# Kernel tuning notes

Hardware: AMD Instinct MI355X
Metric: run time of the kernel (lower is better)

Reference implementation:

```python
import jax, jax.numpy as jnp
import numpy as np

K = 6  # knn_number
EPS_CS = 1e-8  # F.cosine_similarity eps


def _sqdist(a, b):
    # a: [B,N,3], b: [B,M,3] -> [B,N,M] squared euclidean distances
    return (jnp.sum(a * a, -1)[:, :, None]
            + jnp.sum(b * b, -1)[:, None, :]
            - 2.0 * jnp.einsum('bnc,bmc->bnm', a, b))


def _batch_norm(x):
    # normalize last dim with the module's exact epsilons
    n = jnp.sqrt(jnp.sum(x * x, axis=-1, keepdims=True) + 1e-08)
    return x / (n + 1e-10)


def _cossim(a, b):
    # torch F.cosine_similarity semantics along last dim
    na = jnp.maximum(jnp.sqrt(jnp.sum(a * a, -1)), EPS_CS)
    nb = jnp.maximum(jnp.sqrt(jnp.sum(b * b, -1)), EPS_CS)
    return jnp.sum(a * b, -1) / (na * nb)


def _gather(points, idx):
    # points: [B,N,C], idx: [B,...] int -> [B,...,C]
    return jax.vmap(lambda p, i: p[i])(points, idx)


def _avg_ori(group_ori, group_nor, batch_ori, batch_nor):
    # group_*: [B,N,K,3], batch_*: [B,N,3]
    nor_diff = jnp.sum(group_nor * batch_nor[:, :, None, :], axis=3)  # [B,N,K]
    nor_diff = jnp.exp(-nor_diff / 0.3) * 10.0 + 1.0
    nor_diff = jnp.where(nor_diff < 4.0, 1.0, 5.0)
    batch_ori_rot = jnp.cross(batch_ori, batch_nor)  # get_ori_rot90: ori x nor
    cos0 = _cossim(group_ori, batch_ori[:, :, None, :])       # [B,N,K]
    cos1 = _cossim(group_ori, batch_ori_rot[:, :, None, :])   # [B,N,K]
    cos = jnp.minimum(1.0 - jnp.abs(cos0), 1.0 - jnp.abs(cos1))
    return jnp.mean(nor_diff * cos)


def _forward(ori_pre, nor_pre, xyz_up, xyz_offset, pts, gt):
    ori_pre = _batch_norm(ori_pre)
    nor_pre = _batch_norm(nor_pre)
    xyz_gt = gt[:, :, 0:3]
    xyz_nor = gt[:, :, 3:6]

    # ori-loss: NN of pts in gt, gather gt normals
    index = jnp.argmin(_sqdist(pts, xyz_gt), axis=2)  # [B,N]
    nor_gt = _gather(xyz_nor, index)                  # [B,N,3]
    d_n = jnp.sum(nor_gt * ori_pre, axis=2, keepdims=True)
    ori_pro = _batch_norm(ori_pre - nor_gt * d_n)

    # smooth field over KNN (self-knn over pts, includes self)
    idx = jax.lax.top_k(-_sqdist(pts, pts), K)[1]  # [B,N,K]
    group_ori = _gather(ori_pro, idx)              # [B,N,K,3]
    group_nor = _gather(nor_gt, idx)
    loss_smooth = _avg_ori(group_ori, group_nor, ori_pro, nor_gt)

    # normal estimation loss
    loss_nor = jnp.mean(1.0 - jnp.abs(_cossim(nor_gt, nor_pre)))

    # chamfer distances (squared-dist chamfer)
    do = _sqdist(xyz_offset, xyz_gt)
    loss_charm_offset = jnp.mean(jnp.min(do, axis=2)) + jnp.mean(jnp.min(do, axis=1))
    du = _sqdist(xyz_up, xyz_gt)
    loss_charm = jnp.mean(jnp.min(du, axis=2)) + jnp.mean(jnp.min(du, axis=1))

    # nor-ori orthogonality
    loss_nor_ori = jnp.mean(jnp.abs(jnp.sum(ori_pre * nor_gt, axis=2)))

    loss_cd = loss_charm + 0.4 * loss_charm_offset
    loss = loss_smooth + loss_nor + 0.1 * loss_nor_ori + 200.0 * loss_cd
    return (loss, loss_smooth, loss_nor, loss_charm_offset, loss_nor_ori, loss_charm, loss_charm)


def setup_inputs() -> dict:
    key = jax.random.key(0)
    k = jax.random.split(key, 6)
    B, N, NG, NU = 4, 4096, 4096, 8192
    gt_xyz = jax.random.normal(k[5], (B, NG, 3), dtype=jnp.float32)
    gt_nor = _batch_norm(jax.random.normal(jax.random.fold_in(key, 7), (B, NG, 3), dtype=jnp.float32))
    return {
        'ori_pre': jax.random.normal(k[0], (B, N, 3), dtype=jnp.float32),
        'nor_pre': jax.random.normal(k[1], (B, N, 3), dtype=jnp.float32),
        'xyz_up': jax.random.normal(k[2], (B, NU, 3), dtype=jnp.float32),
        'xyz_offset': jax.random.normal(k[3], (B, NU, 3), dtype=jnp.float32),
        'pts': jax.random.normal(k[4], (B, N, 3), dtype=jnp.float32),
        'gt': jnp.concatenate([gt_xyz, gt_nor], axis=-1),
        'epoch': 1,
    }


def reference(ori_pre, nor_pre, xyz_up, xyz_offset, pts, gt, epoch):
    # epoch is unused by the original forward as well
    return _forward(ori_pre, nor_pre, xyz_up, xyz_offset, pts, gt)
```

## Files before the change

### kernel.cpp

```cpp
#include <hip/hip_runtime.h>
#include <stdint.h>

#define NN 4096
#define NGG 4096
#define NUU 8192

__device__ __forceinline__ unsigned fkey32(float f) {
  unsigned u = __float_as_uint(f);
  return u ^ (((int)u >> 31) | 0x80000000u);
}
__device__ __forceinline__ float unfkey32(unsigned k) {
  unsigned m = (k & 0x80000000u) ? 0x80000000u : 0xFFFFFFFFu;
  return __uint_as_float(k ^ m);
}

__device__ __forceinline__ float block_sum_256(float v, float* sbuf) {
#pragma unroll
  for (int o = 32; o > 0; o >>= 1) v += __shfl_down(v, o, 64);
  int lane = threadIdx.x & 63;
  int w = threadIdx.x >> 6;
  if (lane == 0) sbuf[w] = v;
  __syncthreads();
  float r = 0.f;
  if (threadIdx.x == 0) r = sbuf[0] + sbuf[1] + sbuf[2] + sbuf[3];
  __syncthreads();
  return r;
}

__device__ __forceinline__ float block_sum_512(float v, float* sbuf) {
#pragma unroll
  for (int o = 32; o > 0; o >>= 1) v += __shfl_down(v, o, 64);
  int lane = threadIdx.x & 63;
  int w = threadIdx.x >> 6;
  if (lane == 0) sbuf[w] = v;
  __syncthreads();
  float r = 0.f;
  if (threadIdx.x == 0) {
#pragma unroll
    for (int i = 0; i < 8; ++i) r += sbuf[i];
  }
  __syncthreads();
  return r;
}

__global__ __launch_bounds__(256) void k_scan(const float* __restrict__ pts,
                                              const float* __restrict__ gt,
                                              const float* __restrict__ up,
                                              const float* __restrict__ off,
                                              unsigned long long* __restrict__ keys,
                                              unsigned* __restrict__ rowmin,
                                              unsigned* __restrict__ colmin,
                                              float* __restrict__ acc) {
  __shared__ float4 sc[512];
  int blk = blockIdx.x;
  int tid = threadIdx.x;
  if (blk == 0 && tid < 16) acc[tid] = 0.f;

  if (blk < 512) {
    int qb = blk >> 3;
    int seg = blk & 7;
    int wb = qb >> 3;
    int which = wb >> 2;
    int b = wb & 3;
    int r0 = (qb & 7) * 1024 + tid * 4;
    {
      const float* gtb = gt + (size_t)b * NGG * 6 + (size_t)seg * 512 * 6;
      int i0 = tid * 2;
      const float4* g4 = (const float4*)(gtb + (size_t)i0 * 6);
      float4 u0 = g4[0], u1 = g4[1], u2 = g4[2];
      sc[i0] = make_float4(u0.x, u0.y, u0.z,
                           fmaf(u0.x, u0.x, fmaf(u0.y, u0.y, u0.z * u0.z)));
      sc[i0 + 1] = make_float4(u1.z, u1.w, u2.x,
                               fmaf(u1.z, u1.z, fmaf(u1.w, u1.w, u2.x * u2.x)));
    }
    const float* src = which ? up : off;
    const float4* s4 = (const float4*)src;
    size_t fb = ((size_t)(b * NUU + r0) * 3) >> 2;
    float4 A = s4[fb], B = s4[fb + 1], C = s4[fb + 2];
    float q0x = A.x, q0y = A.y, q0z = A.z;
    float q1x = A.w, q1y = B.x, q1z = B.y;
    float q2x = B.z, q2y = B.w, q2z = C.x;
    float q3x = C.y, q3y = C.z, q3z = C.w;
    float qq0 = fmaf(q0x, q0x, fmaf(q0y, q0y, q0z * q0z));
    float qq1 = fmaf(q1x, q1x, fmaf(q1y, q1y, q1z * q1z));
    float qq2 = fmaf(q2x, q2x, fmaf(q2y, q2y, q2z * q2z));
    float qq3 = fmaf(q3x, q3x, fmaf(q3y, q3y, q3z * q3z));
    float a0x = -2.f * q0x, a0y = -2.f * q0y, a0z = -2.f * q0z;
    float a1x = -2.f * q1x, a1y = -2.f * q1y, a1z = -2.f * q1z;
    float a2x = -2.f * q2x, a2y = -2.f * q2y, a2z = -2.f * q2z;
    float a3x = -2.f * q3x, a3y = -2.f * q3y, a3z = -2.f * q3z;
    __syncthreads();
    float b0 = 3.4e38f, b1 = 3.4e38f, b2 = 3.4e38f, b3 = 3.4e38f;
#pragma unroll 4
    for (int j = 0; j < 512; ++j) {
      float4 c = sc[j];
      float t;
      t = fmaf(c.x, a0x, c.w); t = fmaf(c.y, a0y, t); t = fmaf(c.z, a0z, t); b0 = fminf(b0, t);
      t = fmaf(c.x, a1x, c.w); t = fmaf(c.y, a1y, t); t = fmaf(c.z, a1z, t); b1 = fminf(b1, t);
      t = fmaf(c.x, a2x, c.w); t = fmaf(c.y, a2y, t); t = fmaf(c.z, a2z, t); b2 = fminf(b2, t);
      t = fmaf(c.x, a3x, c.w); t = fmaf(c.y, a3y, t); t = fmaf(c.z, a3z, t); b3 = fminf(b3, t);
    }
    int gr = which * 32768 + b * NUU + r0;
    atomicMin(&rowmin[gr + 0], fkey32(b0 + qq0));
    atomicMin(&rowmin[gr + 1], fkey32(b1 + qq1));
    atomicMin(&rowmin[gr + 2], fkey32(b2 + qq2));
    atomicMin(&rowmin[gr + 3], fkey32(b3 + qq3));

  } else if (blk < 1024) {
    int blk2 = blk - 512;
    int qb = blk2 >> 4;
    int seg = blk2 & 15;
    int which = qb >> 4;
    int b = (qb >> 2) & 3;
    int m0 = (qb & 3) * 1024 + tid * 4;
    const float* src = which ? up : off;
    if (tid < 128) {
      const float* sb = src + (size_t)b * NUU * 3 + (size_t)seg * 512 * 3;
      int i0 = tid * 4;
      const float4* s4 = (const float4*)(sb + (size_t)i0 * 3);
      float4 u0 = s4[0], u1 = s4[1], u2 = s4[2];
      sc[i0] = make_float4(u0.x, u0.y, u0.z,
                           fmaf(u0.x, u0.x, fmaf(u0.y, u0.y, u0.z * u0.z)));
      sc[i0 + 1] = make_float4(u0.w, u1.x, u1.y,
                               fmaf(u0.w, u0.w, fmaf(u1.x, u1.x, u1.y * u1.y)));
      sc[i0 + 2] = make_float4(u1.z, u1.w, u2.x,
                               fmaf(u1.z, u1.z, fmaf(u1.w, u1.w, u2.x * u2.x)));
      sc[i0 + 3] = make_float4(u2.y, u2.z, u2.w,
                               fmaf(u2.y, u2.y, fmaf(u2.z, u2.z, u2.w * u2.w)));
    }
    const float* g = gt + (size_t)b * NGG * 6 + (size_t)m0 * 6;
    float q0x = g[0],  q0y = g[1],  q0z = g[2];
    float q1x = g[6],  q1y = g[7],  q1z = g[8];
    float q2x = g[12], q2y = g[13], q2z = g[14];
    float q3x = g[18], q3y = g[19], q3z = g[20];
    float qq0 = fmaf(q0x, q0x, fmaf(q0y, q0y, q0z * q0z));
    float qq1 = fmaf(q1x, q1x, fmaf(q1y, q1y, q1z * q1z));
    float qq2 = fmaf(q2x, q2x, fmaf(q2y, q2y, q2z * q2z));
    float qq3 = fmaf(q3x, q3x, fmaf(q3y, q3y, q3z * q3z));
    float a0x = -2.f * q0x, a0y = -2.f * q0y, a0z = -2.f * q0z;
    float a1x = -2.f * q1x, a1y = -2.f * q1y, a1z = -2.f * q1z;
    float a2x = -2.f * q2x, a2y = -2.f * q2y, a2z = -2.f * q2z;
    float a3x = -2.f * q3x, a3y = -2.f * q3y, a3z = -2.f * q3z;
    __syncthreads();
    float b0 = 3.4e38f, b1 = 3.4e38f, b2 = 3.4e38f, b3 = 3.4e38f;
#pragma unroll 4
    for (int j = 0; j < 512; ++j) {
      float4 c = sc[j];
      float t;
      t = fmaf(c.x, a0x, c.w); t = fmaf(c.y, a0y, t); t = fmaf(c.z, a0z, t); b0 = fminf(b0, t);
      t = fmaf(c.x, a1x, c.w); t = fmaf(c.y, a1y, t); t = fmaf(c.z, a1z, t); b1 = fminf(b1, t);
      t = fmaf(c.x, a2x, c.w); t = fmaf(c.y, a2y, t); t = fmaf(c.z, a2z, t); b2 = fminf(b2, t);
      t = fmaf(c.x, a3x, c.w); t = fmaf(c.y, a3y, t); t = fmaf(c.z, a3z, t); b3 = fminf(b3, t);
    }
    int gc = which * 16384 + b * NGG + m0;
    atomicMin(&colmin[gc + 0], fkey32(b0 + qq0));
    atomicMin(&colmin[gc + 1], fkey32(b1 + qq1));
    atomicMin(&colmin[gc + 2], fkey32(b2 + qq2));
    atomicMin(&colmin[gc + 3], fkey32(b3 + qq3));

  } else {
    int blk3 = blk - 1024;
    int qb = blk3 >> 4;
    int seg = blk3 & 15;
    int b = qb >> 2;
    int m0 = (qb & 3) * 1024 + tid * 4;
    if (tid < 128) {
      const float* gtb = gt + (size_t)b * NGG * 6 + (size_t)seg * 256 * 6;
      int i0 = tid * 2;
      const float4* g4 = (const float4*)(gtb + (size_t)i0 * 6);
      float4 u0 = g4[0], u1 = g4[1], u2 = g4[2];
      sc[i0] = make_float4(u0.x, u0.y, u0.z,
                           fmaf(u0.x, u0.x, fmaf(u0.y, u0.y, u0.z * u0.z)));
      sc[i0 + 1] = make_float4(u1.z, u1.w, u2.x,
                               fmaf(u1.z, u1.z, fmaf(u1.w, u1.w, u2.x * u2.x)));
    }
    size_t fb = ((size_t)(b * NN + m0) * 3) >> 2;
    const float4* p4 = (const float4*)pts;
    float4 A = p4[fb], B = p4[fb + 1], C = p4[fb + 2];
    float q0x = A.x, q0y = A.y, q0z = A.z;
    float q1x = A.w, q1y = B.x, q1z = B.y;
    float q2x = B.z, q2y = B.w, q2z = C.x;
    float q3x = C.y, q3y = C.z, q3z = C.w;
    float a0x = -2.f * q0x, a0y = -2.f * q0y, a0z = -2.f * q0z;
    float a1x = -2.f * q1x, a1y = -2.f * q1y, a1z = -2.f * q1z;
    float a2x = -2.f * q2x, a2y = -2.f * q2y, a2z = -2.f * q2z;
    float a3x = -2.f * q3x, a3y = -2.f * q3y, a3z = -2.f * q3z;
    __syncthreads();
    float b0 = 3.4e38f, b1 = 3.4e38f, b2 = 3.4e38f, b3 = 3.4e38f;
    int i0 = 0, i1 = 0, i2 = 0, i3 = 0;
#pragma unroll 4
    for (int j = 0; j < 256; ++j) {
      float4 c = sc[j];
      float t; bool cc;
      t = fmaf(c.x, a0x, c.w); t = fmaf(c.y, a0y, t); t = fmaf(c.z, a0z, t);
      cc = t < b0; b0 = cc ? t : b0; i0 = cc ? j : i0;
      t = fmaf(c.x, a1x, c.w); t = fmaf(c.y, a1y, t); t = fmaf(c.z, a1z, t);
      cc = t < b1; b1 = cc ? t : b1; i1 = cc ? j : i1;
      t = fmaf(c.x, a2x, c.w); t = fmaf(c.y, a2y, t); t = fmaf(c.z, a2z, t);
      cc = t < b2; b2 = cc ? t : b2; i2 = cc ? j : i2;
      t = fmaf(c.x, a3x, c.w); t = fmaf(c.y, a3y, t); t = fmaf(c.z, a3z, t);
      cc = t < b3; b3 = cc ? t : b3; i3 = cc ? j : i3;
    }
    int q = b * NN + m0;
    int base = seg * 256;
    atomicMin(&keys[q + 0], ((unsigned long long)fkey32(b0) << 32) | (unsigned)(base + i0));
    atomicMin(&keys[q + 1], ((unsigned long long)fkey32(b1) << 32) | (unsigned)(base + i1));
    atomicMin(&keys[q + 2], ((unsigned long long)fkey32(b2) << 32) | (unsigned)(base + i2));
    atomicMin(&keys[q + 3], ((unsigned long long)fkey32(b3) << 32) | (unsigned)(base + i3));
  }
}

__global__ __launch_bounds__(256) void k_post(
    const float* __restrict__ ori_pre, const float* __restrict__ nor_pre,
    const float* __restrict__ gt, const unsigned long long* __restrict__ keys,
    const unsigned* __restrict__ rowmin, const unsigned* __restrict__ colmin,
    float* __restrict__ nor_gt, float* __restrict__ ori_pro, float* __restrict__ acc) {
  __shared__ float sb1[4], sb2[4];
  int blk = blockIdx.x;
  if (blk < 64) {
    int q = blk * 256 + threadIdx.x;
    int b = q >> 12;
    float ox = ori_pre[q * 3 + 0], oy = ori_pre[q * 3 + 1], oz = ori_pre[q * 3 + 2];
    float n1 = sqrtf(fmaf(ox, ox, fmaf(oy, oy, oz * oz)) + 1e-8f) + 1e-10f;
    ox /= n1; oy /= n1; oz /= n1;
    float px = nor_pre[q * 3 + 0], py = nor_pre[q * 3 + 1], pz = nor_pre[q * 3 + 2];
    float n2 = sqrtf(fmaf(px, px, fmaf(py, py, pz * pz)) + 1e-8f) + 1e-10f;
    px /= n2; py /= n2; pz /= n2;
    unsigned idx = (unsigned)(keys[q] & 0xffffffffULL);
    const float* g = gt + (size_t)b * NGG * 6 + (size_t)idx * 6 + 3;
    float gx = g[0], gy = g[1], gz = g[2];
    float dn = fmaf(gx, ox, fmaf(gy, oy, gz * oz));
    float vx = ox - gx * dn, vy = oy - gy * dn, vz = oz - gz * dn;
    float n3 = sqrtf(fmaf(vx, vx, fmaf(vy, vy, vz * vz)) + 1e-8f) + 1e-10f;
    vx /= n3; vy /= n3; vz /= n3;
    nor_gt[q * 3 + 0] = gx; nor_gt[q * 3 + 1] = gy; nor_gt[q * 3 + 2] = gz;
    ori_pro[q * 3 + 0] = vx; ori_pro[q * 3 + 1] = vy; ori_pro[q * 3 + 2] = vz;
    float na = fmaxf(sqrtf(fmaf(gx, gx, fmaf(gy, gy, gz * gz))), 1e-8f);
    float nb = fmaxf(sqrtf(fmaf(px, px, fmaf(py, py, pz * pz))), 1e-8f);
    float cs = fmaf(gx, px, fmaf(gy, py, gz * pz)) / (na * nb);
    float t_nor = 1.f - fabsf(cs);
    float t_ori = fabsf(dn);
    float s1 = block_sum_256(t_nor, sb1);
    float s2 = block_sum_256(t_ori, sb2);
    if (threadIdx.x == 0) {
      atomicAdd(&acc[1], s1);
      atomicAdd(&acc[2], s2);
    }
  } else {
    int rblk = blk - 64;
    float v;
    int slot;
    if (rblk < 256) {
      int i = rblk * 256 + threadIdx.x;
      v = unfkey32(rowmin[i]);
      slot = (i >> 15) ? 5 : 3;
    } else {
      int i = (rblk - 256) * 256 + threadIdx.x;
      v = unfkey32(colmin[i]);
      slot = (i >> 14) ? 6 : 4;
    }
    float s = block_sum_256(v, sb1);
    if (threadIdx.x == 0) atomicAdd(&acc[slot], s);
  }
}

#define INSERT6(D, CI)                                                          \
  {                                                                             \
    float d_ = (D); int ci_ = (CI);                                             \
    bool cc; float nd; int ni;                                                  \
    cc = d_ < d0; nd = cc ? d_ : d0; d_ = cc ? d0 : d_; ni = cc ? ci_ : i0; ci_ = cc ? i0 : ci_; d0 = nd; i0 = ni; \
    cc = d_ < d1; nd = cc ? d_ : d1; d_ = cc ? d1 : d_; ni = cc ? ci_ : i1; ci_ = cc ? i1 : ci_; d1 = nd; i1 = ni; \
    cc = d_ < d2; nd = cc ? d_ : d2; d_ = cc ? d2 : d_; ni = cc ? ci_ : i2; ci_ = cc ? i2 : ci_; d2 = nd; i2 = ni; \
    cc = d_ < d3; nd = cc ? d_ : d3; d_ = cc ? d3 : d_; ni = cc ? ci_ : i3; ci_ = cc ? i3 : ci_; d3 = nd; i3 = ni; \
    cc = d_ < d4; nd = cc ? d_ : d4; d_ = cc ? d4 : d_; ni = cc ? ci_ : i4; ci_ = cc ? i4 : ci_; d4 = nd; i4 = ni; \
    cc = d_ < d5; nd = cc ? d_ : d5;                    ni = cc ? ci_ : i5;                      d5 = nd; i5 = ni; \
  }

__global__ __launch_bounds__(512, 8) void k_knn_smooth(const float* __restrict__ pts,
                                                       const float* __restrict__ nor_gt,
                                                       const float* __restrict__ ori_pro,
                                                       float* __restrict__ acc,
                                                       float* __restrict__ out) {
  __shared__ float4 sp[1152];
  __shared__ float sbuf[8];
  int tid = threadIdx.x;
  int q_local = tid >> 5;
  int t = tid & 31;
  int q = blockIdx.x * 16 + q_local;
  int b = q >> 12;
  int n = q & 4095;
  const float* pb = pts + (size_t)b * NN * 3;
  float qx = pb[n * 3 + 0], qy = pb[n * 3 + 1], qz = pb[n * 3 + 2];
  float qx2 = -2.f * qx, qy2 = -2.f * qy, qz2 = -2.f * qz;
  float d0 = 3.4e38f, d1 = 3.4e38f, d2 = 3.4e38f,
        d3 = 3.4e38f, d4 = 3.4e38f, d5 = 3.4e38f;
  int i0 = 0, i1 = 0, i2 = 0, i3 = 0, i4 = 0, i5 = 0;
  int toff = t + (t >> 3);

  for (int ch = 0; ch < 4; ++ch) {
    if (tid < 256) {
      const float4* p4 = (const float4*)(pb + (size_t)(ch * 1024 + tid * 4) * 3);
      float4 u0 = p4[0], u1 = p4[1], u2 = p4[2];
      int il = tid * 4;
      int si = il + (il >> 3);
      sp[si] = make_float4(u0.x, u0.y, u0.z,
                           fmaf(u0.x, u0.x, fmaf(u0.y, u0.y, u0.z * u0.z)));
      sp[si + 1] = make_float4(u0.w, u1.x, u1.y,
                               fmaf(u0.w, u0.w, fmaf(u1.x, u1.x, u1.y * u1.y)));
      sp[si + 2] = make_float4(u1.z, u1.w, u2.x,
                               fmaf(u1.z, u1.z, fmaf(u1.w, u1.w, u2.x * u2.x)));
      sp[si + 3] = make_float4(u2.y, u2.z, u2.w,
                               fmaf(u2.y, u2.y, fmaf(u2.z, u2.z, u2.w * u2.w)));
    }
    __syncthreads();
    int cbase = ch << 10;
    for (int jo = 0; jo < 4; ++jo) {
      float T = d5;
#pragma unroll
      for (int o = 16; o > 0; o >>= 1) T = fminf(T, __shfl_xor(T, o, 32));
#pragma unroll
      for (int ji = 0; ji < 2; ++ji) {
        int c0 = (((jo << 1) | ji) << 7) | t;
        int s0 = c0 + (c0 >> 3);
        float4 p0 = sp[s0];
        float4 p1 = sp[s0 + 36];
        float4 p2 = sp[s0 + 72];
        float4 p3 = sp[s0 + 108];
        float da = fmaf(p0.x, qx2, p0.w); da = fmaf(p0.y, qy2, da); da = fmaf(p0.z, qz2, da);
        float db = fmaf(p1.x, qx2, p1.w); db = fmaf(p1.y, qy2, db); db = fmaf(p1.z, qz2, db);
        float dc = fmaf(p2.x, qx2, p2.w); dc = fmaf(p2.y, qy2, dc); dc = fmaf(p2.z, qz2, dc);
        float dd = fmaf(p3.x, qx2, p3.w); dd = fmaf(p3.y, qy2, dd); dd = fmaf(p3.z, qz2, dd);
        float mmin = fminf(fminf(da, db), fminf(dc, dd));
        if (mmin <= T) {
          int cg = cbase | c0;
          if (da <= T) INSERT6(da, cg)
          if (db <= T) INSERT6(db, cg + 32)
          if (dc <= T) INSERT6(dc, cg + 64)
          if (dd <= T) INSERT6(dd, cg + 96)
        }
      }
    }
    __syncthreads();
  }
  (void)toff;

  int myid = 0;
#pragma unroll
  for (int r = 0; r < 6; ++r) {
    unsigned long long h = ((unsigned long long)fkey32(d0) << 32) | (unsigned)i0;
    unsigned long long m = h;
#pragma unroll
    for (int o = 16; o > 0; o >>= 1) {
      unsigned long long other = __shfl_xor(m, o, 32);
      m = (other < m) ? other : m;
    }
    if (t == r) myid = (int)(m & 0xffffffffULL);
    if (h == m) {
      d0 = d1; i0 = i1; d1 = d2; i1 = i2; d2 = d3; i2 = i3;
      d3 = d4; i3 = i4; d4 = d5; i4 = i5; d5 = 3.4e38f;
    }
  }

  float sum = 0.f;
  if (t < 6) {
    const float* gq = nor_gt + (size_t)q * 3;
    float ngx = gq[0], ngy = gq[1], ngz = gq[2];
    const float* oq = ori_pro + (size_t)q * 3;
    float box = oq[0], boy = oq[1], boz = oq[2];
    float rx = boy * ngz - boz * ngy;
    float ry = boz * ngx - box * ngz;
    float rz = box * ngy - boy * ngx;
    float nbo = fmaxf(sqrtf(fmaf(box, box, fmaf(boy, boy, boz * boz))), 1e-8f);
    float nrot = fmaxf(sqrtf(fmaf(rx, rx, fmaf(ry, ry, rz * rz))), 1e-8f);
    const float* gn = nor_gt + (size_t)(b * 4096 + myid) * 3;
    const float* go = ori_pro + (size_t)(b * 4096 + myid) * 3;
    float gnx = gn[0], gny = gn[1], gnz = gn[2];
    float gox = go[0], goy = go[1], goz = go[2];
    float ndv = fmaf(gnx, ngx, fmaf(gny, ngy, gnz * ngz));
    float wv = (expf(-ndv / 0.3f) * 10.f + 1.f) < 4.f ? 1.f : 5.f;
    float ngo = fmaxf(sqrtf(fmaf(gox, gox, fmaf(goy, goy, goz * goz))), 1e-8f);
    float c0 = fmaf(gox, box, fmaf(goy, boy, goz * boz)) / (ngo * nbo);
    float c1 = fmaf(gox, rx, fmaf(goy, ry, goz * rz)) / (ngo * nrot);
    float cosv = fminf(1.f - fabsf(c0), 1.f - fabsf(c1));
    sum = wv * cosv;
  }
  float s = block_sum_512(sum, sbuf);

  if (tid == 0) {
    atomicAdd(&acc[0], s);
    __threadfence();
    unsigned c = atomicAdd((unsigned*)(acc + 9), 1u);
    if (c == gridDim.x - 1) {
      __threadfence();
      float a0 = atomicAdd(&acc[0], 0.f);
      float a1 = atomicAdd(&acc[1], 0.f);
      float a2 = atomicAdd(&acc[2], 0.f);
      float a3 = atomicAdd(&acc[3], 0.f);
      float a4 = atomicAdd(&acc[4], 0.f);
      float a5 = atomicAdd(&acc[5], 0.f);
      float a6 = atomicAdd(&acc[6], 0.f);
      float loss_smooth = a0 / 98304.f;
      float loss_nor = a1 / 16384.f;
      float loss_nor_ori = a2 / 16384.f;
      float lco = a3 / 32768.f + a4 / 16384.f;
      float lc = a5 / 32768.f + a6 / 16384.f;
      float loss_cd = lc + 0.4f * lco;
      float loss = loss_smooth + loss_nor + 0.1f * loss_nor_ori + 200.f * loss_cd;
      out[0] = loss;
      out[1] = loss_smooth;
      out[2] = loss_nor;
      out[3] = lco;
      out[4] = loss_nor_ori;
      out[5] = lc;
      out[6] = lc;
    }
  }
}

extern "C" void kernel_launch(void* const* d_in, const int* in_sizes, int n_in,
                              void* d_out, int out_size, void* d_ws, size_t ws_size,
                              hipStream_t stream) {
  (void)in_sizes; (void)n_in; (void)out_size; (void)ws_size;
  const float* ori_pre = (const float*)d_in[0];
  const float* nor_pre = (const float*)d_in[1];
  const float* xyz_up = (const float*)d_in[2];
  const float* xyz_off = (const float*)d_in[3];
  const float* pts = (const float*)d_in[4];
  const float* gt = (const float*)d_in[5];
  float* out = (float*)d_out;
  char* ws = (char*)d_ws;

  float* acc = (float*)(ws + 0);
  unsigned long long* keys = (unsigned long long*)(ws + 512);
  unsigned* rowmin = (unsigned*)(ws + 512 + 131072);
  unsigned* colmin = (unsigned*)(ws + 512 + 131072 + 262144);
  float* nor_gt = (float*)(ws + 512 + 131072 + 262144 + 131072);
  float* ori_pro = (float*)(ws + 512 + 131072 + 262144 + 131072 + 196608);

  hipMemsetAsync(ws + 512, 0xFF, 131072 + 262144 + 131072, stream);

  k_scan<<<1280, 256, 0, stream>>>(pts, gt, xyz_up, xyz_off, keys, rowmin,
                                   colmin, acc);
  k_post<<<448, 256, 0, stream>>>(ori_pre, nor_pre, gt, keys, rowmin, colmin,
                                  nor_gt, ori_pro, acc);
  k_knn_smooth<<<1024, 512, 0, stream>>>(pts, nor_gt, ori_pro, acc, out);
}
```

Measured before the change: 194.1 us.

## Stage all points in LDS once and prefilter KNN with a two-pass threshold

Loads all 4096 points per batch into shared memory in a single stage instead of four chunked loads with barriers. A first pass computes each lane's minimum distance, and the sixth-smallest of those per-lane minima across the 32 lanes becomes a safe upper bound tau on the true 6th-nearest distance. A second pass then inserts only candidates at or below tau, cutting top-6 insertion work and the per-chunk shuffle threshold updates. The costs are computing every distance twice, a much larger LDS footprint (about 72KB per block), and lower occupancy, with the launch-bounds minimum blocks lowered from 8 to 4.

```diff
diff --git a/kernel.cpp b/kernel.cpp
--- a/kernel.cpp
+++ b/kernel.cpp
@@ -276,12 +276,12 @@
     cc = d_ < d5; nd = cc ? d_ : d5;                    ni = cc ? ci_ : i5;                      d5 = nd; i5 = ni; \
   }
 
-__global__ __launch_bounds__(512, 8) void k_knn_smooth(const float* __restrict__ pts,
+__global__ __launch_bounds__(512, 4) void k_knn_smooth(const float* __restrict__ pts,
                                                        const float* __restrict__ nor_gt,
                                                        const float* __restrict__ ori_pro,
                                                        float* __restrict__ acc,
                                                        float* __restrict__ out) {
-  __shared__ float4 sp[1152];
+  __shared__ float4 sp[4608];
   __shared__ float sbuf[8];
   int tid = threadIdx.x;
   int q_local = tid >> 5;
@@ -290,72 +290,96 @@
   int b = q >> 12;
   int n = q & 4095;
   const float* pb = pts + (size_t)b * NN * 3;
+
+  {
+    int il = tid * 8;
+    const float4* p4 = (const float4*)(pb + (size_t)il * 3);
+    float4 u0 = p4[0], u1 = p4[1], u2 = p4[2], u3 = p4[3], u4 = p4[4], u5 = p4[5];
+    int si = il + (il >> 3);
+    sp[si + 0] = make_float4(u0.x, u0.y, u0.z,
+                             fmaf(u0.x, u0.x, fmaf(u0.y, u0.y, u0.z * u0.z)));
+    sp[si + 1] = make_float4(u0.w, u1.x, u1.y,
+                             fmaf(u0.w, u0.w, fmaf(u1.x, u1.x, u1.y * u1.y)));
+    sp[si + 2] = make_float4(u1.z, u1.w, u2.x,
+                             fmaf(u1.z, u1.z, fmaf(u1.w, u1.w, u2.x * u2.x)));
+    sp[si + 3] = make_float4(u2.y, u2.z, u2.w,
+                             fmaf(u2.y, u2.y, fmaf(u2.z, u2.z, u2.w * u2.w)));
+    sp[si + 4] = make_float4(u3.x, u3.y, u3.z,
+                             fmaf(u3.x, u3.x, fmaf(u3.y, u3.y, u3.z * u3.z)));
+    sp[si + 5] = make_float4(u3.w, u4.x, u4.y,
+                             fmaf(u3.w, u3.w, fmaf(u4.x, u4.x, u4.y * u4.y)));
+    sp[si + 6] = make_float4(u4.z, u4.w, u5.x,
+                             fmaf(u4.z, u4.z, fmaf(u4.w, u4.w, u5.x * u5.x)));
+    sp[si + 7] = make_float4(u5.y, u5.z, u5.w,
+                             fmaf(u5.y, u5.y, fmaf(u5.z, u5.z, u5.w * u5.w)));
+  }
+  __syncthreads();
+
   float qx = pb[n * 3 + 0], qy = pb[n * 3 + 1], qz = pb[n * 3 + 2];
   float qx2 = -2.f * qx, qy2 = -2.f * qy, qz2 = -2.f * qz;
+
+  float m = 3.4e38f;
+#pragma unroll 4
+  for (int gg = 0; gg < 32; ++gg) {
+    int c0 = (gg << 7) | t;
+    int s0 = c0 + (c0 >> 3);
+    float4 p0 = sp[s0];
+    float4 p1 = sp[s0 + 36];
+    float4 p2 = sp[s0 + 72];
+    float4 p3 = sp[s0 + 108];
+    float da = fmaf(p0.x, qx2, p0.w); da = fmaf(p0.y, qy2, da); da = fmaf(p0.z, qz2, da);
+    float db = fmaf(p1.x, qx2, p1.w); db = fmaf(p1.y, qy2, db); db = fmaf(p1.z, qz2, db);
+    float dc = fmaf(p2.x, qx2, p2.w); dc = fmaf(p2.y, qy2, dc); dc = fmaf(p2.z, qz2, dc);
+    float dd = fmaf(p3.x, qx2, p3.w); dd = fmaf(p3.y, qy2, dd); dd = fmaf(p3.z, qz2, dd);
+    m = fminf(m, fminf(fminf(da, db), fminf(dc, dd)));
+  }
+
+  float mv = m, tau = 3.4e38f;
+#pragma unroll
+  for (int r = 0; r < 6; ++r) {
+    float w = mv;
+#pragma unroll
+    for (int o = 16; o > 0; o >>= 1) w = fminf(w, __shfl_xor(w, o, 32));
+    tau = w;
+    if (mv == w) mv = 3.4e38f;
+  }
+
   float d0 = 3.4e38f, d1 = 3.4e38f, d2 = 3.4e38f,
         d3 = 3.4e38f, d4 = 3.4e38f, d5 = 3.4e38f;
   int i0 = 0, i1 = 0, i2 = 0, i3 = 0, i4 = 0, i5 = 0;
-  int toff = t + (t >> 3);
-
-  for (int ch = 0; ch < 4; ++ch) {
-    if (tid < 256) {
-      const float4* p4 = (const float4*)(pb + (size_t)(ch * 1024 + tid * 4) * 3);
-      float4 u0 = p4[0], u1 = p4[1], u2 = p4[2];
-      int il = tid * 4;
-      int si = il + (il >> 3);
-      sp[si] = make_float4(u0.x, u0.y, u0.z,
-                           fmaf(u0.x, u0.x, fmaf(u0.y, u0.y, u0.z * u0.z)));
-      sp[si + 1] = make_float4(u0.w, u1.x, u1.y,
-                               fmaf(u0.w, u0.w, fmaf(u1.x, u1.x, u1.y * u1.y)));
-      sp[si + 2] = make_float4(u1.z, u1.w, u2.x,
-                               fmaf(u1.z, u1.z, fmaf(u1.w, u1.w, u2.x * u2.x)));
-      sp[si + 3] = make_float4(u2.y, u2.z, u2.w,
-                               fmaf(u2.y, u2.y, fmaf(u2.z, u2.z, u2.w * u2.w)));
-    }
-    __syncthreads();
-    int cbase = ch << 10;
-    for (int jo = 0; jo < 4; ++jo) {
-      float T = d5;
-#pragma unroll
-      for (int o = 16; o > 0; o >>= 1) T = fminf(T, __shfl_xor(T, o, 32));
-#pragma unroll
-      for (int ji = 0; ji < 2; ++ji) {
-        int c0 = (((jo << 1) | ji) << 7) | t;
-        int s0 = c0 + (c0 >> 3);
-        float4 p0 = sp[s0];
-        float4 p1 = sp[s0 + 36];
-        float4 p2 = sp[s0 + 72];
-        float4 p3 = sp[s0 + 108];
-        float da = fmaf(p0.x, qx2, p0.w); da = fmaf(p0.y, qy2, da); da = fmaf(p0.z, qz2, da);
-        float db = fmaf(p1.x, qx2, p1.w); db = fmaf(p1.y, qy2, db); db = fmaf(p1.z, qz2, db);
-        float dc = fmaf(p2.x, qx2, p2.w); dc = fmaf(p2.y, qy2, dc); dc = fmaf(p2.z, qz2, dc);
-        float dd = fmaf(p3.x, qx2, p3.w); dd = fmaf(p3.y, qy2, dd); dd = fmaf(p3.z, qz2, dd);
-        float mmin = fminf(fminf(da, db), fminf(dc, dd));
-        if (mmin <= T) {
-          int cg = cbase | c0;
-          if (da <= T) INSERT6(da, cg)
-          if (db <= T) INSERT6(db, cg + 32)
-          if (dc <= T) INSERT6(dc, cg + 64)
-          if (dd <= T) INSERT6(dd, cg + 96)
-        }
-      }
-    }
-    __syncthreads();
-  }
-  (void)toff;
+#pragma unroll 2
+  for (int gg = 0; gg < 32; ++gg) {
+    int c0 = (gg << 7) | t;
+    int s0 = c0 + (c0 >> 3);
+    float4 p0 = sp[s0];
+    float4 p1 = sp[s0 + 36];
+    float4 p2 = sp[s0 + 72];
+    float4 p3 = sp[s0 + 108];
+    float da = fmaf(p0.x, qx2, p0.w); da = fmaf(p0.y, qy2, da); da = fmaf(p0.z, qz2, da);
+    float db = fmaf(p1.x, qx2, p1.w); db = fmaf(p1.y, qy2, db); db = fmaf(p1.z, qz2, db);
+    float dc = fmaf(p2.x, qx2, p2.w); dc = fmaf(p2.y, qy2, dc); dc = fmaf(p2.z, qz2, dc);
+    float dd = fmaf(p3.x, qx2, p3.w); dd = fmaf(p3.y, qy2, dd); dd = fmaf(p3.z, qz2, dd);
+    float mmin = fminf(fminf(da, db), fminf(dc, dd));
+    if (mmin <= tau) {
+      if (da <= tau) INSERT6(da, c0)
+      if (db <= tau) INSERT6(db, c0 + 32)
+      if (dc <= tau) INSERT6(dc, c0 + 64)
+      if (dd <= tau) INSERT6(dd, c0 + 96)
+    }
+  }
 
   int myid = 0;
 #pragma unroll
   for (int r = 0; r < 6; ++r) {
     unsigned long long h = ((unsigned long long)fkey32(d0) << 32) | (unsigned)i0;
-    unsigned long long m = h;
+    unsigned long long mk = h;
 #pragma unroll
     for (int o = 16; o > 0; o >>= 1) {
-      unsigned long long other = __shfl_xor(m, o, 32);
-      m = (other < m) ? other : m;
-    }
-    if (t == r) myid = (int)(m & 0xffffffffULL);
-    if (h == m) {
+      unsigned long long other = __shfl_xor(mk, o, 32);
+      mk = (other < mk) ? other : mk;
+    }
+    if (t == r) myid = (int)(mk & 0xffffffffULL);
+    if (h == mk) {
       d0 = d1; i0 = i1; d1 = d2; i1 = i2; d2 = d3; i2 = i3;
       d3 = d4; i3 = i4; d4 = d5; i4 = i5; d5 = 3.4e38f;
     }
```

Measured after the change: 185.5 us. 4.4% less time.
